# Optimization experiments

Hardware: AMD Instinct MI355X
Metric: run time of the kernel (lower is better)

The kernel has to match this reference:

```python
import jax, jax.numpy as jnp
import numpy as np

N = 4096          # num_nodes
E = 131072        # num_edges (avg degree 32)
H = 32            # hidden_channels
C_IN, C_OUT = 3, 3
DEPTH = 4
KS = [2000, 1000, 500, 250]  # ceil(ratio * n) per level, ratios = [2000/N, .5, .5, .5]


def gcn(x, A, W, b):
    """GCNConv with improved=True (self-loop fill 2, preserved if already present),
    symmetric normalization, aggregation out[dst] += norm * h[src]."""
    d = jnp.diagonal(A)
    A_hat = A + jnp.diag(jnp.where(d > 0, 0.0, 2.0))
    deg = A_hat.sum(0)                       # in-degree (col sums), as gcn_norm
    dis = jnp.where(deg > 0, jax.lax.rsqrt(deg), 0.0)
    msg = (x @ W) * dis[:, None]
    return (A_hat.T @ msg) * dis[:, None] + b


def augment(A):
    """GraphUNet.augment_adj: add self loops (w=1), square adjacency, drop self loops."""
    n = A.shape[0]
    eye = jnp.eye(n, dtype=A.dtype)
    A_sl = A + eye
    return (A_sl @ A_sl) * (1.0 - eye)


def pool(x, A, p, k):
    """TopKPooling: score = tanh((x.p)/||p||), keep top-k, gate x by score."""
    score = jnp.tanh((x @ p) / jnp.linalg.norm(p))
    vals, perm = jax.lax.top_k(score, k)
    return x[perm] * vals[:, None], A[perm][:, perm], perm


def setup_inputs() -> dict:
    key = jax.random.key(0)
    ks = jax.random.split(key, 12)
    x = jax.random.normal(ks[0], (N, C_IN), jnp.float32)
    edge_index = jax.random.randint(ks[1], (2, E), 0, N, dtype=jnp.int64)
    s = 0.1
    return {
        "x": x,
        "edge_index": edge_index,
        "W0": jax.random.normal(ks[2], (C_IN, H)) * s,
        "b0": jnp.zeros((H,), jnp.float32),
        "Wd": jax.random.normal(ks[3], (DEPTH, H, H)) * s,
        "bd": jnp.zeros((DEPTH, H), jnp.float32),
        "P": jax.random.normal(ks[4], (DEPTH, H)) * s,
        "Wu": jax.random.normal(ks[5], (DEPTH - 1, H, H)) * s,
        "bu": jnp.zeros((DEPTH - 1, H), jnp.float32),
        "Wlast": jax.random.normal(ks[6], (H, C_OUT)) * s,
        "blast": jnp.zeros((C_OUT,), jnp.float32),
    }


def reference(x, edge_index, W0, b0, Wd, bd, P, Wu, bu, Wlast, blast):
    # dense adjacency; duplicate edges accumulate like coalesced sparse weights
    A = jnp.zeros((N, N), jnp.float32).at[edge_index[0], edge_index[1]].add(1.0)
    x = jax.nn.relu(gcn(x, A, W0, b0))
    xs, As, perms = [x], [A], []
    for i in range(DEPTH):
        A = augment(A)
        x, A, perm = pool(x, A, P[i], KS[i])
        x = jax.nn.relu(gcn(x, A, Wd[i], bd[i]))
        if i < DEPTH - 1:
            xs.append(x)
            As.append(A)
        perms.append(perm)
    for i in range(DEPTH):
        j = DEPTH - 1 - i
        res = xs[j]
        up = jnp.zeros_like(res).at[perms[j]].set(x)  # unpool
        x = res + up                                   # sum_res=True
        if i < DEPTH - 1:
            x = jax.nn.relu(gcn(x, As[j], Wu[i], bu[i]))
        else:
            x = gcn(x, As[j], Wlast, blast)
    return jax.nn.log_softmax(x, axis=1)
```

## Files before the change

### kernel.cpp

```cpp
#include <hip/hip_runtime.h>
#include <math.h>

#define H 32
#define N0 4096
#define EMAX 131072
#define APSTR (4096 * 32)

typedef __attribute__((ext_vector_type(4))) float floatx4;
typedef __attribute__((ext_vector_type(8))) short short8;

__device__ __forceinline__ unsigned short f2bf_bits(float v) {
    union { float f; unsigned u; } c;
    c.f = v;
    unsigned lsb = (c.u >> 16) & 1u;
    c.u += 0x7fffu + lsb;
    return (unsigned short)(c.u >> 16);
}

__device__ __forceinline__ float bf2f(unsigned short u) {
    union { unsigned x; float f; } c;
    c.x = (unsigned)u << 16;
    return c.f;
}

__device__ __forceinline__ float cvtA(float f) { return f; }
__device__ __forceinline__ float cvtA(unsigned short u) { return bf2f(u); }

__global__ void fill_sentinel_kernel(float* out, int n) {
    int t = blockIdx.x * 256 + threadIdx.x;
    if (t < n) out[t] = 9.0f;
}

__global__ void build_stats_kernel(const int* __restrict__ ei, int E, int* __restrict__ rowcnt,
                                   int* __restrict__ rowcntD, int* __restrict__ diagcnt) {
    int t = blockIdx.x * 256 + threadIdx.x;
    if (t >= E) return;
    int s = ei[t], d = ei[E + t];
    if ((unsigned)s >= N0 || (unsigned)d >= N0) return;
    atomicAdd(&rowcnt[s], 1);
    atomicAdd(&rowcntD[d], 1);
    if (s == d) atomicAdd(&diagcnt[s], 1);
}

__global__ __launch_bounds__(1024) void scan2_kernel(const int* __restrict__ cntA, int* __restrict__ rowpA,
                                                     int* __restrict__ curA, const int* __restrict__ cntB,
                                                     int* __restrict__ rowpB, int* __restrict__ curB) {
    __shared__ int wsA[16], wsB[16], weA[16], weB[16];
    int tid = threadIdx.x;
    int lane = tid & 63, wid = tid >> 6;
    int base = tid * 4;
    int lA[4], lB[4];
    int sA = 0, sB = 0;
#pragma unroll
    for (int i = 0; i < 4; i++) { lA[i] = sA; sA += cntA[base + i]; }
#pragma unroll
    for (int i = 0; i < 4; i++) { lB[i] = sB; sB += cntB[base + i]; }
    int iA = sA, iB = sB;
#pragma unroll
    for (int off = 1; off < 64; off <<= 1) {
        int vA = __shfl_up(iA, off);
        int vB = __shfl_up(iB, off);
        if (lane >= off) { iA += vA; iB += vB; }
    }
    if (lane == 63) { wsA[wid] = iA; wsB[wid] = iB; }
    __syncthreads();
    if (tid < 16) {
        int a = wsA[tid], b = wsB[tid];
        int ia = a, ib = b;
#pragma unroll
        for (int off = 1; off < 16; off <<= 1) {
            int va = __shfl_up(ia, off);
            int vb = __shfl_up(ib, off);
            if (tid >= off) { ia += va; ib += vb; }
        }
        weA[tid] = ia - a;
        weB[tid] = ib - b;
    }
    __syncthreads();
    int preA = weA[wid] + iA - sA;
    int preB = weB[wid] + iB - sB;
#pragma unroll
    for (int i = 0; i < 4; i++) {
        int a = preA + lA[i], b = preB + lB[i];
        rowpA[base + i] = a; curA[base + i] = a;
        rowpB[base + i] = b; curB[base + i] = b;
    }
    if (tid == 1023) { rowpA[N0] = preA + sA; rowpB[N0] = preB + sB; }
}

__global__ void fillcsr_msg0_kernel(const int* __restrict__ ei, int E, int* __restrict__ cursor,
                                    int* __restrict__ cols, int* __restrict__ cursorD,
                                    int* __restrict__ srcs, const float* __restrict__ x,
                                    const float* __restrict__ Wb, const int* __restrict__ rcntD,
                                    const int* __restrict__ diagcnt, float* __restrict__ dis,
                                    float* __restrict__ fixb, float* __restrict__ msg, int n) {
    int nf = (E + 255) >> 8;
    int tid = threadIdx.x;
    if ((int)blockIdx.x < nf) {
        int t = blockIdx.x * 256 + tid;
        if (t >= E) return;
        int s = ei[t], d = ei[E + t];
        if ((unsigned)s >= N0 || (unsigned)d >= N0) return;
        int pos = atomicAdd(&cursor[s], 1);
        cols[pos] = d;
        int posD = atomicAdd(&cursorD[d], 1);
        srcs[posD] = s;
    } else {
        int idx = ((int)blockIdx.x - nf) * 256 + tid;
        if (idx >= n * 32) return;
        int i = idx >> 5, c = idx & 31;
        float fx = diagcnt[i] > 0 ? 0.f : 2.f;
        float dg = (float)rcntD[i] + fx;
        float di = dg > 0.f ? 1.f / sqrtf(dg) : 0.f;
        if (c == 0) { dis[i] = di; fixb[i] = fx; }
        float s = x[i * 3] * Wb[c] + x[i * 3 + 1] * Wb[32 + c] + x[i * 3 + 2] * Wb[64 + c];
        msg[idx] = s * di;
    }
}

__global__ __launch_bounds__(256) void aug0_kernel(const int* __restrict__ rowp, const int* __restrict__ cols,
                                                   const int* __restrict__ perm, const int* __restrict__ invperm,
                                                   int kOut, int ldC, unsigned short* __restrict__ C) {
    __shared__ float row[2048];
    int a = blockIdx.x;
    int tid = threadIdx.x;
    for (int j = tid; j < ldC; j += 256) row[j] = 0.f;
    __syncthreads();
    if (a < kOut) {
        int pa = perm[a];
        int s0 = rowp[pa], s1 = rowp[pa + 1];
        int sub = tid & 7, grp = tid >> 3;
        for (int e = s0 + grp; e < s1; e += 32) {
            int k = cols[e];
            if (sub == 0) {
                int ip = invperm[k];
                if (ip >= 0) atomicAdd(&row[ip], 2.0f);
            }
            int t1 = rowp[k + 1];
            for (int e2 = rowp[k] + sub; e2 < t1; e2 += 8) {
                int ip2 = invperm[cols[e2]];
                if (ip2 >= 0) atomicAdd(&row[ip2], 1.0f);
            }
        }
    }
    __syncthreads();
    for (int j = tid; j < ldC; j += 256)
        C[(long)a * ldC + j] = (j == a) ? 0 : f2bf_bits(row[j]);
}

__global__ void gatherAB_bf16_kernel(const unsigned short* __restrict__ M, int ldM,
                                     const int* __restrict__ perm, const int* __restrict__ invp,
                                     int kOut, unsigned short* __restrict__ Gr,
                                     unsigned short* __restrict__ GcT, int ldn,
                                     float* __restrict__ Cz) {
    __shared__ float t[32][33];
    __shared__ int rj[32];
    int half = (ldM >> 8) * ldn;
    int tseg = (ldM >> 5) * (ldM >> 5);
    int zrow = (((ldn - kOut) * ldM) + 255) >> 8;
    int u = blockIdx.x;
    int tid = threadIdx.x;
    if (u < half) {
        int gx = ldM >> 8;
        int a = u / gx;
        int k = (u % gx) * 256 + tid;
        float v = 0.f;
        if (a < kOut) {
            int pa = perm[a];
            v = bf2f(M[(long)pa * ldM + k]) + (k == pa ? 1.f : 0.f);
        }
        Gr[(long)a * ldM + k] = f2bf_bits(v);
    } else if (u < half + tseg) {
        u -= half;
        int ntx = ldM >> 5;
        int bx = u % ntx, by = u / ntx;
        int j0 = bx * 32, k0 = by * 32;
        int tx = tid & 31, ty = tid >> 5;
        if (ty == 0) rj[tx] = invp[j0 + tx];
        __syncthreads();
        for (int y = ty; y < 32; y += 8)
            t[y][tx] = bf2f(M[(long)(k0 + y) * ldM + j0 + tx]);
        __syncthreads();
        for (int y = ty; y < 32; y += 8) {
            int r = rj[y];
            if (r >= 0)
                GcT[(long)r * ldM + k0 + tx] =
                    f2bf_bits(t[tx][y] + ((k0 + tx) == (j0 + y) ? 1.f : 0.f));
        }
    } else if (u < half + tseg + zrow) {
        int e = (u - half - tseg) * 256 + tid;
        if (e < (ldn - kOut) * ldM) GcT[(long)kOut * ldM + e] = 0;
    } else {
        int t4 = (u - half - tseg - zrow) * 256 + tid;
        if (t4 < (ldn * ldn) >> 2) {
            floatx4 z = {0.f, 0.f, 0.f, 0.f};
            ((floatx4*)Cz)[t4] = z;
        }
    }
}

__global__ void gatherGT_kernel(const float* __restrict__ M, int ldM, const int* __restrict__ perm,
                                const int* __restrict__ invp, int kOut,
                                float* __restrict__ Gr, float* __restrict__ GcT, int ldn,
                                float* __restrict__ deg) {
    __shared__ float t[32][33];
    __shared__ int rj[32];
    int half = (ldM >> 8) * ldn;
    int tseg = (ldM >> 5) * (ldM >> 5);
    int zrow = (((ldn - kOut) * ldM) + 255) >> 8;
    int u = blockIdx.x;
    int tid = threadIdx.x;
    if (u < half) {
        int gx = ldM >> 8;
        int a = u / gx;
        int k = (u % gx) * 256 + tid;
        float v = 0.f;
        if (a < kOut) {
            int pa = perm[a];
            v = M[(long)pa * ldM + k] + (k == pa ? 1.f : 0.f);
        }
        Gr[(long)a * ldM + k] = v;
    } else if (u < half + tseg) {
        u -= half;
        int ntx = ldM >> 5;
        int bx = u % ntx, by = u / ntx;
        int j0 = bx * 32, k0 = by * 32;
        int tx = tid & 31, ty = tid >> 5;
        if (ty == 0) rj[tx] = invp[j0 + tx];
        __syncthreads();
        for (int y = ty; y < 32; y += 8)
            t[y][tx] = M[(long)(k0 + y) * ldM + j0 + tx];
        __syncthreads();
        for (int y = ty; y < 32; y += 8) {
            int r = rj[y];
            if (r >= 0)
                GcT[(long)r * ldM + k0 + tx] = t[tx][y] + ((k0 + tx) == (j0 + y) ? 1.f : 0.f);
        }
    } else if (u < half + tseg + zrow) {
        int e = (u - half - tseg) * 256 + tid;
        if (e < (ldn - kOut) * ldM) GcT[(long)kOut * ldM + e] = 0.f;
    } else {
        int tt = (u - half - tseg - zrow) * 256 + tid;
        if (tt < ldn) deg[tt] = 0.f;
    }
}

__global__ __launch_bounds__(256) void mfma_aug_kernel(const unsigned short* __restrict__ Aop,
                                                       const unsigned short* __restrict__ Bop,
                                                       float* __restrict__ C, int K, int ldC, int kchunk) {
    __shared__ __align__(16) unsigned short lA[64 * 32];
    __shared__ __align__(16) unsigned short lB[64 * 32];
    const int tid = threadIdx.x;
    const int lane = tid & 63;
    const int w = tid >> 6;
    const int a0 = blockIdx.y * 64, b0 = blockIdx.x * 64;
    const int kbase = blockIdx.z * kchunk;
    const int r0 = tid >> 2;
    const int c8 = (tid & 3) * 8;
    const unsigned short* gA = Aop + (long)(a0 + r0) * K + kbase + c8;
    const unsigned short* gB = Bop + (long)(b0 + r0) * K + kbase + c8;
    const int wm = (w & 1) * 32;
    const int wn = (w >> 1) * 32;
    const int lm = lane & 15;
    const int quad = lane >> 4;
    floatx4 acc[2][2];
#pragma unroll
    for (int i = 0; i < 2; i++)
#pragma unroll
        for (int j = 0; j < 2; j++) {
            floatx4 z = {0.f, 0.f, 0.f, 0.f};
            acc[i][j] = z;
        }
    for (int k0 = 0; k0 < kchunk; k0 += 32) {
        short8 va = *(const short8*)(gA + k0);
        short8 vb = *(const short8*)(gB + k0);
        __syncthreads();
        *(short8*)&lA[r0 * 32 + c8] = va;
        *(short8*)&lB[r0 * 32 + c8] = vb;
        __syncthreads();
        short8 af[2], bf[2];
#pragma unroll
        for (int mi = 0; mi < 2; mi++) af[mi] = *(const short8*)&lA[(wm + mi * 16 + lm) * 32 + quad * 8];
#pragma unroll
        for (int ni = 0; ni < 2; ni++) bf[ni] = *(const short8*)&lB[(wn + ni * 16 + lm) * 32 + quad * 8];
#pragma unroll
        for (int mi = 0; mi < 2; mi++)
#pragma unroll
            for (int ni = 0; ni < 2; ni++)
                acc[mi][ni] = __builtin_amdgcn_mfma_f32_16x16x32_bf16(af[mi], bf[ni], acc[mi][ni], 0, 0, 0);
    }
#pragma unroll
    for (int mi = 0; mi < 2; mi++)
#pragma unroll
        for (int ni = 0; ni < 2; ni++) {
            int col = b0 + wn + ni * 16 + lm;
#pragma unroll
            for (int r = 0; r < 4; r++) {
                int row = a0 + wm + mi * 16 + quad * 4 + r;
                if (row != col) atomicAdd(&C[(long)row * ldC + col], acc[mi][ni][r]);
            }
        }
}

__global__ __launch_bounds__(256) void gemm64_kernel(const float* __restrict__ Gr,
                                                     const float* __restrict__ GcT,
                                                     float* __restrict__ Cpart, int K, int ldC, int kchunk) {
    __shared__ float As[32][68];
    __shared__ float Bs[32][68];
    const int tid = threadIdx.x;
    const int a0 = blockIdx.y * 64, b0 = blockIdx.x * 64;
    const int kbase = blockIdx.z * kchunk;
    float* Cz = Cpart + (long)blockIdx.z * ldC * ldC;
    const int tx = tid & 15, ty = tid >> 4;
    const int lr = tid >> 2;
    const int lk = (tid & 3) * 8;
    const float* gA = Gr + (long)(a0 + lr) * K + lk + kbase;
    const float* gB = GcT + (long)(b0 + lr) * K + lk + kbase;
    float acc[4][4];
#pragma unroll
    for (int i = 0; i < 4; i++)
#pragma unroll
        for (int j = 0; j < 4; j++) acc[i][j] = 0.f;
    for (int k0 = 0; k0 < kchunk; k0 += 32) {
        float a8[8], b8[8];
#pragma unroll
        for (int i = 0; i < 8; i++) a8[i] = gA[k0 + i];
#pragma unroll
        for (int i = 0; i < 8; i++) b8[i] = gB[k0 + i];
        __syncthreads();
#pragma unroll
        for (int i = 0; i < 8; i++) As[lk + i][lr] = a8[i];
#pragma unroll
        for (int i = 0; i < 8; i++) Bs[lk + i][lr] = b8[i];
        __syncthreads();
#pragma unroll
        for (int k = 0; k < 32; k++) {
            floatx4 av = *(const floatx4*)&As[k][ty * 4];
            floatx4 bv = *(const floatx4*)&Bs[k][tx * 4];
#pragma unroll
            for (int i = 0; i < 4; i++)
#pragma unroll
                for (int j = 0; j < 4; j++) acc[i][j] += av[i] * bv[j];
        }
    }
#pragma unroll
    for (int i = 0; i < 4; i++)
#pragma unroll
        for (int j = 0; j < 4; j++) {
            int a = a0 + ty * 4 + i, b = b0 + tx * 4 + j;
            Cz[(long)a * ldC + b] = acc[i][j];
        }
}

__global__ void reduce_part_deg_kernel(const float* __restrict__ Cpart, float* __restrict__ C,
                                       int ldC, int ksplit, float* __restrict__ deg) {
    int t = blockIdx.x * 256 + threadIdx.x;
    long tot = (long)ldC * ldC;
    if (t >= tot) return;
    float s = 0.f;
    for (int z = 0; z < ksplit; z++) s += Cpart[(long)z * tot + t];
    int a = t / ldC, b = t % ldC;
    if (a == b) s = 0.f;
    C[t] = s;
    if (s != 0.f) atomicAdd(&deg[b], s);
}

template <typename AT>
__global__ void colsum_rawmsg_kernel(const AT* __restrict__ A, int ld, int hascs,
                                     const float* __restrict__ x, const int* __restrict__ perm,
                                     const float* __restrict__ vals, const float* __restrict__ xup,
                                     const int* __restrict__ invp, const float* __restrict__ Wb,
                                     float* __restrict__ degp, float* __restrict__ rm, int n) {
    int nc = hascs ? (ld >> 8) * (ld >> 6) : 0;
    int tid = threadIdx.x;
    if ((int)blockIdx.x < nc) {
        int gx = ld >> 8;
        int bi = blockIdx.x % gx, jb = blockIdx.x / gx;
        int i = bi * 256 + tid;
        int j0 = jb * 64;
        const AT* p = A + (long)j0 * ld + i;
        float s0 = 0.f, s1 = 0.f, s2 = 0.f, s3 = 0.f, s4 = 0.f, s5 = 0.f, s6 = 0.f, s7 = 0.f;
#pragma unroll
        for (int jq = 0; jq < 64; jq += 8) {
            float v[8];
#pragma unroll
            for (int q = 0; q < 8; q++) v[q] = cvtA(p[(long)(jq + q) * ld]);
            s0 += v[0]; s1 += v[1]; s2 += v[2]; s3 += v[3];
            s4 += v[4]; s5 += v[5]; s6 += v[6]; s7 += v[7];
        }
        float s = ((s0 + s1) + (s2 + s3)) + ((s4 + s5) + (s6 + s7));
        degp[(long)jb * ld + i] = s;
    } else {
        int idx = ((int)blockIdx.x - nc) * 256 + tid;
        if (idx >= ld * 32) return;
        int i = idx >> 5, c = idx & 31;
        float v = 0.f;
        if (i < n) {
            int src = perm ? perm[i] : i;
            float vs = vals ? vals[i] : 1.f;
            int ip = invp ? invp[i] : -1;
            float s = 0.f;
#pragma unroll
            for (int q = 0; q < 32; q++) {
                float xv = x[(long)src * 32 + q];
                if (ip >= 0) xv += xup[(long)ip * 32 + q];
                s += xv * Wb[q * 32 + c];
            }
            v = s * vs;
        }
        rm[idx] = v;
    }
}

template <typename AT>
__global__ __launch_bounds__(256) void aggTs_kernel(const AT* __restrict__ A,
                                                    const float* __restrict__ rm,
                                                    const float* __restrict__ degp, int nparts,
                                                    const float* __restrict__ disC,
                                                    float* __restrict__ aggp, int n, int ld, int jchunk) {
    __shared__ float As[64][64];
    __shared__ float Ms[64][32];
    __shared__ float sdisJ[256];
    const int tid = threadIdx.x;
    const int i0 = blockIdx.x * 64;
    const int j0 = blockIdx.y * jchunk;
    for (int j = tid; j < jchunk; j += 256) {
        int jj = j0 + j;
        float d;
        if (nparts) {
            float s = 0.f;
            for (int z = 0; z < nparts; z++) s += degp[(long)z * ld + jj];
            d = 1.f / sqrtf(s + 2.f);
        } else {
            d = disC[jj];
        }
        sdisJ[j] = d;
    }
    __syncthreads();
    const int il = tid & 63;
    const int cg = tid >> 6;
    const int i = i0 + il;
    const int mrow = tid >> 2;
    const int mc = (tid & 3) * 8;
    float acc[8];
#pragma unroll
    for (int q = 0; q < 8; q++) acc[q] = 0.f;
    for (int jb = j0; jb < j0 + jchunk; jb += 64) {
        AT a16[16];
        float m8[8];
#pragma unroll
        for (int q = 0; q < 16; q++) a16[q] = A[(long)(jb + cg + 4 * q) * ld + i0 + il];
#pragma unroll
        for (int q = 0; q < 8; q++) m8[q] = rm[(long)(jb + mrow) * 32 + mc + q];
        __syncthreads();
#pragma unroll
        for (int q = 0; q < 16; q++) As[cg + 4 * q][il] = cvtA(a16[q]);
        float ds = sdisJ[jb - j0 + mrow];
#pragma unroll
        for (int q = 0; q < 8; q++) Ms[mrow][mc + q] = m8[q] * ds;
        __syncthreads();
#pragma unroll
        for (int jl = 0; jl < 64; jl++) {
            float a = As[jl][il];
#pragma unroll
            for (int q = 0; q < 8; q++) acc[q] += a * Ms[jl][cg * 8 + q];
        }
        __syncthreads();
    }
    if (i < n) {
#pragma unroll
        for (int q = 0; q < 8; q++) aggp[(long)blockIdx.y * APSTR + (long)i * 32 + cg * 8 + q] = acc[q];
    }
}

__global__ void epi2_kernel(const float* __restrict__ aggp, int jsplit, const float* __restrict__ rm,
                            const float* __restrict__ degp, int nparts, float* __restrict__ disC,
                            int writeDis, int ld, const float* __restrict__ bb,
                            float* __restrict__ out, int n, const float* __restrict__ p, int npow,
                            unsigned long long* __restrict__ keys) {
    __shared__ float psh[32];
    if (p) {
        if (threadIdx.x < 32) psh[threadIdx.x] = p[threadIdx.x];
        __syncthreads();
    }
    int idx = blockIdx.x * 256 + threadIdx.x;
    int tot = (p ? npow : n) * 32;
    if (idx >= tot) return;
    int i = idx >> 5, c = idx & 31;
    float di;
    if (nparts) {
        float s = 0.f;
        for (int z = 0; z < nparts; z++) s += degp[(long)z * ld + i];
        di = 1.f / sqrtf(s + 2.f);
    } else {
        di = disC[i];
    }
    float v = 0.f;
    if (i < n) {
        float s = 0.f;
        for (int z = 0; z < jsplit; z++) s += aggp[(long)z * APSTR + idx];
        v = (s + 2.f * di * rm[idx]) * di + bb[c];
        v = fmaxf(v, 0.f);
        out[idx] = v;
    }
    if (writeDis && c == 0) disC[i] = di;
    if (p) {
        float pc = psh[c];
        float d = v * pc;
        float nq = pc * pc;
#pragma unroll
        for (int st = 16; st >= 1; st >>= 1) {
            d += __shfl_xor(d, st);
            nq += __shfl_xor(nq, st);
        }
        if (c == 0) {
            unsigned long long kk = 0ULL;
            if (i < n) {
                float sc = tanhf(d / sqrtf(nq));
                unsigned u = __float_as_uint(sc);
                u = (u & 0x80000000u) ? ~u : (u | 0x80000000u);
                kk = ((unsigned long long)u << 32) | (unsigned)(~i);
            }
            keys[i] = kk;
        }
    }
}

__global__ void cscagg_epi_keys_kernel(const int* __restrict__ rowpD, const int* __restrict__ srcs,
                                       const float* __restrict__ msg, const float* __restrict__ dis,
                                       const float* __restrict__ fixb, const float* __restrict__ bb,
                                       float* __restrict__ out, int n, const float* __restrict__ p,
                                       unsigned long long* __restrict__ keys) {
    __shared__ float psh[32];
    if (threadIdx.x < 32) psh[threadIdx.x] = p[threadIdx.x];
    __syncthreads();
    int idx = blockIdx.x * 256 + threadIdx.x;
    if (idx >= n * 32) return;
    int i = idx >> 5, c = idx & 31;
    float acc = 0.f;
    int e0 = rowpD[i], e1 = rowpD[i + 1];
    for (int e = e0; e < e1; e++) acc += msg[(long)srcs[e] * 32 + c];
    float v = (acc + fixb[i] * msg[idx]) * dis[i] + bb[c];
    v = fmaxf(v, 0.f);
    out[idx] = v;
    float pc = psh[c];
    float d = v * pc;
    float nq = pc * pc;
#pragma unroll
    for (int st = 16; st >= 1; st >>= 1) {
        d += __shfl_xor(d, st);
        nq += __shfl_xor(nq, st);
    }
    if (c == 0) {
        float sc = tanhf(d / sqrtf(nq));
        unsigned u = __float_as_uint(sc);
        u = (u & 0x80000000u) ? ~u : (u | 0x80000000u);
        keys[i] = ((unsigned long long)u << 32) | (unsigned)(~i);
    }
}

__global__ void msg3up_kernel(const float* __restrict__ res, const float* __restrict__ xup,
                              const int* __restrict__ invp, const float* __restrict__ Wb,
                              const float* __restrict__ dis, float* __restrict__ msg, int n) {
    int idx = blockIdx.x * 256 + threadIdx.x;
    if (idx >= n * 3) return;
    int i = idx / 3, c = idx % 3;
    int ip = invp[i];
    float s = 0.f;
#pragma unroll
    for (int q = 0; q < 32; q++) {
        float xv = res[(long)i * 32 + q];
        if (ip >= 0) xv += xup[(long)ip * 32 + q];
        s += xv * Wb[q * 3 + c];
    }
    msg[idx] = s * dis[i];
}

__global__ void cscagg_lsm_kernel(const int* __restrict__ rowpD, const int* __restrict__ srcs,
                                  const float* __restrict__ msg, const float* __restrict__ dis,
                                  const float* __restrict__ fixb, const float* __restrict__ bb,
                                  float* __restrict__ out, int n) {
    int i = blockIdx.x * 256 + threadIdx.x;
    if (i >= n) return;
    float a0 = 0.f, a1 = 0.f, a2 = 0.f;
    int e0 = rowpD[i], e1 = rowpD[i + 1];
    for (int e = e0; e < e1; e++) {
        const float* m = &msg[(long)srcs[e] * 3];
        a0 += m[0]; a1 += m[1]; a2 += m[2];
    }
    float di = dis[i], fx = fixb[i];
    float v0 = (a0 + fx * msg[i * 3]) * di + bb[0];
    float v1 = (a1 + fx * msg[i * 3 + 1]) * di + bb[1];
    float v2 = (a2 + fx * msg[i * 3 + 2]) * di + bb[2];
    float m = fmaxf(v0, fmaxf(v1, v2));
    float s = expf(v0 - m) + expf(v1 - m) + expf(v2 - m);
    float l = m + logf(s);
    out[i * 3] = v0 - l;
    out[i * 3 + 1] = v1 - l;
    out[i * 3 + 2] = v2 - l;
}

__global__ __launch_bounds__(256) void topk_rank_kernel(const unsigned long long* __restrict__ keys,
                                                        int npow, int k, int* __restrict__ perm,
                                                        float* __restrict__ vals,
                                                        int* __restrict__ invperm) {
    __shared__ unsigned long long ks[4096];
    __shared__ int psum[256];
    const int tid = threadIdx.x;
    for (int t = tid; t < npow; t += 256) ks[t] = keys[t];
    __syncthreads();
    const int m = tid & 15;
    const int chunk = tid >> 4;
    const int myi = blockIdx.x * 16 + m;
    unsigned long long my = ks[myi];
    const int cl = npow >> 4;
    const unsigned long long* base = &ks[chunk * cl];
    int r = 0;
#pragma unroll 4
    for (int j = 0; j < cl; j++) r += (base[j] > my) ? 1 : 0;
    psum[chunk * 16 + m] = r;
    __syncthreads();
    if (tid < 16) {
        int mk_i = blockIdx.x * 16 + tid;
        unsigned long long mk = ks[mk_i];
        int rank = 0;
#pragma unroll
        for (int c = 0; c < 16; c++) rank += psum[c * 16 + tid];
        invperm[mk_i] = (rank < k) ? rank : -1;
        if (rank < k) {
            perm[rank] = (int)(~(unsigned)mk);
            unsigned u = (unsigned)(mk >> 32);
            u = (u & 0x80000000u) ? (u ^ 0x80000000u) : ~u;
            vals[rank] = __uint_as_float(u);
        }
    }
}

static void run_dense(hipStream_t st, const void* A, int abf, int n, int ld, const float* x,
                      const int* perm, const float* vals, const float* xup, const int* invp,
                      const float* Wt, const float* bt, float* out,
                      float* degp, int nparts, int hascs, float* disC, int writeDis,
                      float* aggp, float* rm,
                      const float* pnext, int npow, unsigned long long* keys) {
    {
        int nc = hascs ? (ld >> 8) * (ld >> 6) : 0;
        int g = nc + (ld * 32 + 255) / 256;
        if (abf)
            colsum_rawmsg_kernel<unsigned short><<<g, 256, 0, st>>>(
                (const unsigned short*)A, ld, hascs, x, perm, vals, xup, invp, Wt, degp, rm, n);
        else
            colsum_rawmsg_kernel<float><<<g, 256, 0, st>>>(
                (const float*)A, ld, hascs, x, perm, vals, xup, invp, Wt, degp, rm, n);
    }
    int jsplit = (ld >= 256) ? (ld >> 8) : 1;
    if (jsplit < 1) jsplit = 1;
    int jchunk = ld / jsplit;
    dim3 ga(ld / 64, jsplit);
    if (abf)
        aggTs_kernel<unsigned short><<<ga, 256, 0, st>>>((const unsigned short*)A, rm,
                                                         nparts ? degp : nullptr, nparts, disC,
                                                         aggp, n, ld, jchunk);
    else
        aggTs_kernel<float><<<ga, 256, 0, st>>>((const float*)A, rm, nparts ? degp : nullptr,
                                                nparts, disC, aggp, n, ld, jchunk);
    int gme = ((pnext ? npow : n) * 32 + 255) / 256;
    epi2_kernel<<<gme, 256, 0, st>>>(aggp, jsplit, rm, nparts ? degp : nullptr, nparts, disC,
                                     writeDis, ld, bt, out, n, pnext, npow, keys);
}

extern "C" void kernel_launch(void* const* d_in, const int* in_sizes, int n_in,
                              void* d_out, int out_size, void* d_ws, size_t ws_size,
                              hipStream_t stream) {
    const float* x0f = (const float*)d_in[0];
    const int* eidx = (const int*)d_in[1];
    const float* W0f = (const float*)d_in[2];
    const float* b0f = (const float*)d_in[3];
    const float* Wdf = (const float*)d_in[4];
    const float* bdf = (const float*)d_in[5];
    const float* Pf = (const float*)d_in[6];
    const float* Wuf = (const float*)d_in[7];
    const float* buf2 = (const float*)d_in[8];
    const float* Wlf = (const float*)d_in[9];
    const float* blf = (const float*)d_in[10];
    const int E = in_sizes[1] / 2;

    unsigned char* w = (unsigned char*)d_ws;
    size_t off = 0;
    auto alloc = [&](size_t bytes) -> void* {
        void* p = w + off;
        off += (bytes + 255) & ~(size_t)255;
        return p;
    };
    int* rowcnt = (int*)alloc(N0 * 4);
    int* rowcntD = (int*)alloc(N0 * 4);
    int* diagcnt = (int*)alloc(N0 * 4);
    int* rowp = (int*)alloc((N0 + 1) * 4);
    int* rowpD = (int*)alloc((N0 + 1) * 4);
    int* cursor = (int*)alloc(N0 * 4);
    int* cursorD = (int*)alloc(N0 * 4);
    int* cols = (int*)alloc((size_t)EMAX * 4);
    int* srcs = (int*)alloc((size_t)EMAX * 4);
    float* dis0 = (float*)alloc(N0 * 4);
    float* fixb0 = (float*)alloc(N0 * 4);
    unsigned long long* keys = (unsigned long long*)alloc((size_t)N0 * 8);
    unsigned short* A1 = (unsigned short*)alloc((size_t)2048 * 2048 * 2);
    float* A2 = (float*)alloc((size_t)1024 * 1024 * 4);
    float* A3 = (float*)alloc((size_t)512 * 512 * 4);
    float* A4 = (float*)alloc((size_t)256 * 256 * 4);
    float* Gr = (float*)alloc((size_t)1024 * 2048 * 4);
    float* Gc = (float*)alloc((size_t)2048 * 1024 * 4);
    unsigned short* Grb = (unsigned short*)alloc((size_t)1024 * 2048 * 2);
    unsigned short* GcTb = (unsigned short*)alloc((size_t)1024 * 2048 * 2);
    float* Cpart = (float*)alloc((size_t)8 * 512 * 512 * 4);
    float* degp = (float*)alloc((size_t)32 * 2048 * 4);
    float* aggp = (float*)alloc((size_t)8 * APSTR * 4);
    float* xs0 = (float*)alloc((size_t)N0 * H * 4);
    float* xs1 = (float*)alloc((size_t)2000 * H * 4);
    float* xs2 = (float*)alloc((size_t)1000 * H * 4);
    float* xs3 = (float*)alloc((size_t)500 * H * 4);
    float* xtB = (float*)alloc((size_t)N0 * H * 4);
    float* xtC = (float*)alloc((size_t)N0 * H * 4);
    float* msgb = (float*)alloc((size_t)N0 * H * 4);
    float* disL = (float*)alloc((size_t)4 * N0 * 4);
    int* invpermL = (int*)alloc((size_t)4 * N0 * 4);
    const int ksz[4] = {2000, 1000, 500, 250};
    int* perm[4];
    float* vals[4];
    for (int i = 0; i < 4; i++) perm[i] = (int*)alloc((size_t)ksz[i] * 4);
    for (int i = 0; i < 4; i++) vals[i] = (float*)alloc((size_t)ksz[i] * 4);

    if (off > ws_size) {
        fill_sentinel_kernel<<<(out_size + 255) / 256, 256, 0, stream>>>((float*)d_out, out_size);
        return;
    }

    const int nlvl[5] = {N0, 2000, 1000, 500, 250};
    const int ldl[5] = {N0, 2048, 1024, 512, 256};
    const int npw[4] = {4096, 2048, 1024, 512};
    void* Afp[5] = {nullptr, A1, A2, A3, A4};
    const int abfL[5] = {0, 1, 0, 0, 0};
    float* xsb[4] = {xs0, xs1, xs2, xs3};

    hipMemsetAsync(rowcnt, 0, (size_t)N0 * 3 * 4, stream);
    build_stats_kernel<<<(E + 255) / 256, 256, 0, stream>>>(eidx, E, rowcnt, rowcntD, diagcnt);
    scan2_kernel<<<1, 1024, 0, stream>>>(rowcnt, rowp, cursor, rowcntD, rowpD, cursorD);
    {
        int nf = (E + 255) / 256;
        int nm = (N0 * H + 255) / 256;
        fillcsr_msg0_kernel<<<nf + nm, 256, 0, stream>>>(eidx, E, cursor, cols, cursorD, srcs,
                                                         x0f, W0f, rowcntD, diagcnt, dis0, fixb0,
                                                         msgb, N0);
    }
    cscagg_epi_keys_kernel<<<(N0 * H + 255) / 256, 256, 0, stream>>>(rowpD, srcs, msgb, dis0, fixb0,
                                                                     b0f, xs0, N0, Pf, keys);
    float* xcur = xs0;

    for (int i = 0; i < 4; ++i) {
        int kk = ksz[i], ldn = ldl[i + 1];
        topk_rank_kernel<<<npw[i] / 16, 256, 0, stream>>>(keys, npw[i], kk, perm[i], vals[i],
                                                          invpermL + i * N0);
        if (i == 0) {
            aug0_kernel<<<ldn, 256, 0, stream>>>(rowp, cols, perm[0], invpermL, kk, ldn, A1);
        } else if (i == 1) {
            int ldM = ldl[i];
            int half = (ldM >> 8) * ldn;
            int tseg = (ldM >> 5) * (ldM >> 5);
            int zrow = (((ldn - kk) * ldM) + 255) >> 8;
            int zseg = ((ldn * ldn) / 4 + 255) / 256;
            gatherAB_bf16_kernel<<<half + tseg + zrow + zseg, 256, 0, stream>>>(
                A1, ldM, perm[i], invpermL + i * N0, kk, Grb, GcTb, ldn, A2);
            int ksplit = 2;
            int kchunk = ldM / ksplit;
            dim3 gg(ldn / 64, ldn / 64, ksplit);
            mfma_aug_kernel<<<gg, 256, 0, stream>>>(Grb, GcTb, A2, ldM, ldn, kchunk);
        } else {
            int ldM = ldl[i];
            int half = (ldM >> 8) * ldn;
            int tseg = (ldM >> 5) * (ldM >> 5);
            int zrow = (((ldn - kk) * ldM) + 255) >> 8;
            int dseg = (ldn + 255) / 256;
            gatherGT_kernel<<<half + tseg + zrow + dseg, 256, 0, stream>>>(
                (const float*)Afp[i], ldM, perm[i], invpermL + i * N0, kk, Gr, Gc, ldn, degp);
            int ksplit = 8;
            int kchunk = ldM / ksplit;
            dim3 gg(ldn / 64, ldn / 64, ksplit);
            gemm64_kernel<<<gg, 256, 0, stream>>>(Gr, Gc, Cpart, ldM, ldn, kchunk);
            long tot = (long)ldn * ldn;
            reduce_part_deg_kernel<<<(tot + 255) / 256, 256, 0, stream>>>(Cpart, (float*)Afp[i + 1],
                                                                          ldn, ksplit, degp);
        }
        float* outx = (i < 3) ? xsb[i + 1] : xtB;
        const float* pnext = (i < 3) ? (Pf + (i + 1) * H) : nullptr;
        int npown = (i < 3) ? npw[i + 1] : 0;
        int hascs = (i <= 1) ? 1 : 0;
        int nparts = (i <= 1) ? (ldn >> 6) : 1;
        run_dense(stream, Afp[i + 1], abfL[i + 1], kk, ldn, xcur, perm[i], vals[i], nullptr,
                  nullptr, Wdf + i * (H * H), bdf + i * H, outx, degp, nparts, hascs,
                  disL + i * N0, (i < 3) ? 1 : 0, aggp, msgb, pnext, npown, keys);
        xcur = outx;
    }

    for (int i = 0; i < 4; ++i) {
        int j = 3 - i;
        int nj = nlvl[j];
        if (i < 3) {
            int ldn = ldl[j];
            float* outx = (xcur == xtB) ? xtC : xtB;
            run_dense(stream, Afp[j], abfL[j], nj, ldn, xsb[j], nullptr, nullptr, xcur,
                      invpermL + j * N0, Wuf + i * (H * H), buf2 + i * H, outx, nullptr, 0, 0,
                      disL + (j - 1) * N0, 0, aggp, msgb, nullptr, 0, nullptr);
            xcur = outx;
        } else {
            msg3up_kernel<<<(N0 * 3 + 255) / 256, 256, 0, stream>>>(xs0, xcur, invpermL, Wlf, dis0,
                                                                    msgb, N0);
            cscagg_lsm_kernel<<<(N0 + 255) / 256, 256, 0, stream>>>(rowpD, srcs, msgb, dis0, fixb0,
                                                                    blf, (float*)d_out, N0);
        }
    }
}
```

Before: 421.1 us.

## Fuse row gather into augment GEMMs and replace split-K reduce with atomics

The augment GEMMs now read rows of the previous adjacency directly through the perm index, adding the self-loop inside the load, so the gathered row matrix Gr/Grb no longer has to be materialised. For levels 2-3 the split-K partial buffer and the separate reduce kernel are dropped. Instead the GEMM atomically accumulates into a pre-zeroed output and computes per-column degree partials in shared memory. This saves a kernel launch and a round trip through memory per level, at the cost of atomic contention and a non-deterministic summation order.

New measurement: 432.6 us. 2.7% more time.

```diff
diff --git a/kernel.cpp b/kernel.cpp
--- a/kernel.cpp
+++ b/kernel.cpp
@@ -148,30 +148,17 @@
         C[(long)a * ldC + j] = (j == a) ? 0 : f2bf_bits(row[j]);
 }
 
-__global__ void gatherAB_bf16_kernel(const unsigned short* __restrict__ M, int ldM,
-                                     const int* __restrict__ perm, const int* __restrict__ invp,
-                                     int kOut, unsigned short* __restrict__ Gr,
-                                     unsigned short* __restrict__ GcT, int ldn,
-                                     float* __restrict__ Cz) {
+__global__ void gatherABt_bf16_kernel(const unsigned short* __restrict__ M, int ldM,
+                                      const int* __restrict__ invp, int kOut,
+                                      unsigned short* __restrict__ GcT, int ldn,
+                                      float* __restrict__ Cz) {
     __shared__ float t[32][33];
     __shared__ int rj[32];
-    int half = (ldM >> 8) * ldn;
     int tseg = (ldM >> 5) * (ldM >> 5);
     int zrow = (((ldn - kOut) * ldM) + 255) >> 8;
     int u = blockIdx.x;
     int tid = threadIdx.x;
-    if (u < half) {
-        int gx = ldM >> 8;
-        int a = u / gx;
-        int k = (u % gx) * 256 + tid;
-        float v = 0.f;
-        if (a < kOut) {
-            int pa = perm[a];
-            v = bf2f(M[(long)pa * ldM + k]) + (k == pa ? 1.f : 0.f);
-        }
-        Gr[(long)a * ldM + k] = f2bf_bits(v);
-    } else if (u < half + tseg) {
-        u -= half;
+    if (u < tseg) {
         int ntx = ldM >> 5;
         int bx = u % ntx, by = u / ntx;
         int j0 = bx * 32, k0 = by * 32;
@@ -187,11 +174,11 @@
                 GcT[(long)r * ldM + k0 + tx] =
                     f2bf_bits(t[tx][y] + ((k0 + tx) == (j0 + y) ? 1.f : 0.f));
         }
-    } else if (u < half + tseg + zrow) {
-        int e = (u - half - tseg) * 256 + tid;
+    } else if (u < tseg + zrow) {
+        int e = (u - tseg) * 256 + tid;
         if (e < (ldn - kOut) * ldM) GcT[(long)kOut * ldM + e] = 0;
     } else {
-        int t4 = (u - half - tseg - zrow) * 256 + tid;
+        int t4 = (u - tseg - zrow) * 256 + tid;
         if (t4 < (ldn * ldn) >> 2) {
             floatx4 z = {0.f, 0.f, 0.f, 0.f};
             ((floatx4*)Cz)[t4] = z;
@@ -199,29 +186,18 @@
     }
 }
 
-__global__ void gatherGT_kernel(const float* __restrict__ M, int ldM, const int* __restrict__ perm,
-                                const int* __restrict__ invp, int kOut,
-                                float* __restrict__ Gr, float* __restrict__ GcT, int ldn,
-                                float* __restrict__ deg) {
+__global__ void gatherT_kernel(const float* __restrict__ M, int ldM,
+                               const int* __restrict__ invp, int kOut,
+                               float* __restrict__ GcT, int ldn,
+                               float* __restrict__ Cz, float* __restrict__ deg) {
     __shared__ float t[32][33];
     __shared__ int rj[32];
-    int half = (ldM >> 8) * ldn;
     int tseg = (ldM >> 5) * (ldM >> 5);
     int zrow = (((ldn - kOut) * ldM) + 255) >> 8;
+    int zcseg = ((ldn * ldn) / 4 + 255) / 256;
     int u = blockIdx.x;
     int tid = threadIdx.x;
-    if (u < half) {
-        int gx = ldM >> 8;
-        int a = u / gx;
-        int k = (u % gx) * 256 + tid;
-        float v = 0.f;
-        if (a < kOut) {
-            int pa = perm[a];
-            v = M[(long)pa * ldM + k] + (k == pa ? 1.f : 0.f);
-        }
-        Gr[(long)a * ldM + k] = v;
-    } else if (u < half + tseg) {
-        u -= half;
+    if (u < tseg) {
         int ntx = ldM >> 5;
         int bx = u % ntx, by = u / ntx;
         int j0 = bx * 32, k0 = by * 32;
@@ -236,16 +212,23 @@
             if (r >= 0)
                 GcT[(long)r * ldM + k0 + tx] = t[tx][y] + ((k0 + tx) == (j0 + y) ? 1.f : 0.f);
         }
-    } else if (u < half + tseg + zrow) {
-        int e = (u - half - tseg) * 256 + tid;
+    } else if (u < tseg + zrow) {
+        int e = (u - tseg) * 256 + tid;
         if (e < (ldn - kOut) * ldM) GcT[(long)kOut * ldM + e] = 0.f;
+    } else if (u < tseg + zrow + zcseg) {
+        int t4 = (u - tseg - zrow) * 256 + tid;
+        if (t4 < (ldn * ldn) >> 2) {
+            floatx4 z = {0.f, 0.f, 0.f, 0.f};
+            ((floatx4*)Cz)[t4] = z;
+        }
     } else {
-        int tt = (u - half - tseg - zrow) * 256 + tid;
+        int tt = (u - tseg - zrow - zcseg) * 256 + tid;
         if (tt < ldn) deg[tt] = 0.f;
     }
 }
 
-__global__ __launch_bounds__(256) void mfma_aug_kernel(const unsigned short* __restrict__ Aop,
+__global__ __launch_bounds__(256) void mfma_aug_kernel(const unsigned short* __restrict__ A1,
+                                                       const int* __restrict__ perm, int kOut,
                                                        const unsigned short* __restrict__ Bop,
                                                        float* __restrict__ C, int K, int ldC, int kchunk) {
     __shared__ __align__(16) unsigned short lA[64 * 32];
@@ -257,7 +240,9 @@
     const int kbase = blockIdx.z * kchunk;
     const int r0 = tid >> 2;
     const int c8 = (tid & 3) * 8;
-    const unsigned short* gA = Aop + (long)(a0 + r0) * K + kbase + c8;
+    const int arow = a0 + r0;
+    const int pa = (arow < kOut) ? perm[arow] : -1;
+    const unsigned short* gA = A1 + (pa >= 0 ? (long)pa * K : 0) + kbase + c8;
     const unsigned short* gB = Bop + (long)(b0 + r0) * K + kbase + c8;
     const int wm = (w & 1) * 32;
     const int wn = (w >> 1) * 32;
@@ -272,7 +257,18 @@
             acc[i][j] = z;
         }
     for (int k0 = 0; k0 < kchunk; k0 += 32) {
-        short8 va = *(const short8*)(gA + k0);
+        short8 va;
+        if (pa >= 0) {
+            va = *(const short8*)(gA + k0);
+            int cb = kbase + c8 + k0;
+            if (pa >= cb && pa < cb + 8) {
+                int e = pa - cb;
+                va[e] = (short)f2bf_bits(bf2f((unsigned short)va[e]) + 1.0f);
+            }
+        } else {
+            short8 z = {0, 0, 0, 0, 0, 0, 0, 0};
+            va = z;
+        }
         short8 vb = *(const short8*)(gB + k0);
         __syncthreads();
         *(short8*)&lA[r0 * 32 + c8] = va;
@@ -302,19 +298,22 @@
         }
 }
 
-__global__ __launch_bounds__(256) void gemm64_kernel(const float* __restrict__ Gr,
-                                                     const float* __restrict__ GcT,
-                                                     float* __restrict__ Cpart, int K, int ldC, int kchunk) {
+__global__ __launch_bounds__(256) void gemm64_atomic_kernel(const float* __restrict__ A,
+                                                            const int* __restrict__ perm, int kOut,
+                                                            const float* __restrict__ GcT,
+                                                            float* __restrict__ C, float* __restrict__ deg,
+                                                            int K, int ldC, int kchunk) {
     __shared__ float As[32][68];
     __shared__ float Bs[32][68];
     const int tid = threadIdx.x;
     const int a0 = blockIdx.y * 64, b0 = blockIdx.x * 64;
     const int kbase = blockIdx.z * kchunk;
-    float* Cz = Cpart + (long)blockIdx.z * ldC * ldC;
     const int tx = tid & 15, ty = tid >> 4;
     const int lr = tid >> 2;
     const int lk = (tid & 3) * 8;
-    const float* gA = Gr + (long)(a0 + lr) * K + lk + kbase;
+    const int arow = a0 + lr;
+    const int pa = (arow < kOut) ? perm[arow] : -1;
+    const float* gA = A + (pa >= 0 ? (long)pa * K : 0) + lk + kbase;
     const float* gB = GcT + (long)(b0 + lr) * K + lk + kbase;
     float acc[4][4];
 #pragma unroll
@@ -323,8 +322,15 @@
         for (int j = 0; j < 4; j++) acc[i][j] = 0.f;
     for (int k0 = 0; k0 < kchunk; k0 += 32) {
         float a8[8], b8[8];
-#pragma unroll
-        for (int i = 0; i < 8; i++) a8[i] = gA[k0 + i];
+        if (pa >= 0) {
+#pragma unroll
+            for (int i = 0; i < 8; i++) a8[i] = gA[k0 + i];
+            int cb = kbase + lk + k0;
+            if (pa >= cb && pa < cb + 8) a8[pa - cb] += 1.f;
+        } else {
+#pragma unroll
+            for (int i = 0; i < 8; i++) a8[i] = 0.f;
+        }
 #pragma unroll
         for (int i = 0; i < 8; i++) b8[i] = gB[k0 + i];
         __syncthreads();
@@ -343,26 +349,28 @@
                 for (int j = 0; j < 4; j++) acc[i][j] += av[i] * bv[j];
         }
     }
+    __syncthreads();
+    float* cps = &As[0][0];
+    float cloc[4] = {0.f, 0.f, 0.f, 0.f};
 #pragma unroll
     for (int i = 0; i < 4; i++)
 #pragma unroll
         for (int j = 0; j < 4; j++) {
             int a = a0 + ty * 4 + i, b = b0 + tx * 4 + j;
-            Cz[(long)a * ldC + b] = acc[i][j];
-        }
-}
-
-__global__ void reduce_part_deg_kernel(const float* __restrict__ Cpart, float* __restrict__ C,
-                                       int ldC, int ksplit, float* __restrict__ deg) {
-    int t = blockIdx.x * 256 + threadIdx.x;
-    long tot = (long)ldC * ldC;
-    if (t >= tot) return;
-    float s = 0.f;
-    for (int z = 0; z < ksplit; z++) s += Cpart[(long)z * tot + t];
-    int a = t / ldC, b = t % ldC;
-    if (a == b) s = 0.f;
-    C[t] = s;
-    if (s != 0.f) atomicAdd(&deg[b], s);
+            float v = acc[i][j];
+            if (a != b) {
+                if (v != 0.f) atomicAdd(&C[(long)a * ldC + b], v);
+                cloc[j] += v;
+            }
+        }
+#pragma unroll
+    for (int j = 0; j < 4; j++) cps[ty * 68 + tx * 4 + j] = cloc[j];
+    __syncthreads();
+    if (tid < 64) {
+        float s = 0.f;
+        for (int t = 0; t < 16; t++) s += cps[t * 68 + tid];
+        if (s != 0.f) atomicAdd(&deg[b0 + tid], s);
+    }
 }
 
 template <typename AT>
@@ -707,11 +715,8 @@
     float* A2 = (float*)alloc((size_t)1024 * 1024 * 4);
     float* A3 = (float*)alloc((size_t)512 * 512 * 4);
     float* A4 = (float*)alloc((size_t)256 * 256 * 4);
-    float* Gr = (float*)alloc((size_t)1024 * 2048 * 4);
     float* Gc = (float*)alloc((size_t)2048 * 1024 * 4);
-    unsigned short* Grb = (unsigned short*)alloc((size_t)1024 * 2048 * 2);
     unsigned short* GcTb = (unsigned short*)alloc((size_t)1024 * 2048 * 2);
-    float* Cpart = (float*)alloc((size_t)8 * 512 * 512 * 4);
     float* degp = (float*)alloc((size_t)32 * 2048 * 4);
     float* aggp = (float*)alloc((size_t)8 * APSTR * 4);
     float* xs0 = (float*)alloc((size_t)N0 * H * 4);
@@ -763,31 +768,30 @@
             aug0_kernel<<<ldn, 256, 0, stream>>>(rowp, cols, perm[0], invpermL, kk, ldn, A1);
         } else if (i == 1) {
             int ldM = ldl[i];
-            int half = (ldM >> 8) * ldn;
             int tseg = (ldM >> 5) * (ldM >> 5);
             int zrow = (((ldn - kk) * ldM) + 255) >> 8;
             int zseg = ((ldn * ldn) / 4 + 255) / 256;
-            gatherAB_bf16_kernel<<<half + tseg + zrow + zseg, 256, 0, stream>>>(
-                A1, ldM, perm[i], invpermL + i * N0, kk, Grb, GcTb, ldn, A2);
+            gatherABt_bf16_kernel<<<tseg + zrow + zseg, 256, 0, stream>>>(
+                A1, ldM, invpermL + i * N0, kk, GcTb, ldn, A2);
             int ksplit = 2;
             int kchunk = ldM / ksplit;
             dim3 gg(ldn / 64, ldn / 64, ksplit);
-            mfma_aug_kernel<<<gg, 256, 0, stream>>>(Grb, GcTb, A2, ldM, ldn, kchunk);
+            mfma_aug_kernel<<<gg, 256, 0, stream>>>(A1, perm[i], kk, GcTb, A2, ldM, ldn, kchunk);
         } else {
             int ldM = ldl[i];
-            int half = (ldM >> 8) * ldn;
             int tseg = (ldM >> 5) * (ldM >> 5);
             int zrow = (((ldn - kk) * ldM) + 255) >> 8;
+            int zcseg = ((ldn * ldn) / 4 + 255) / 256;
             int dseg = (ldn + 255) / 256;
-            gatherGT_kernel<<<half + tseg + zrow + dseg, 256, 0, stream>>>(
-                (const float*)Afp[i], ldM, perm[i], invpermL + i * N0, kk, Gr, Gc, ldn, degp);
+            gatherT_kernel<<<tseg + zrow + zcseg + dseg, 256, 0, stream>>>(
+                (const float*)Afp[i], ldM, invpermL + i * N0, kk, Gc, ldn,
+                (float*)Afp[i + 1], degp);
             int ksplit = 8;
             int kchunk = ldM / ksplit;
             dim3 gg(ldn / 64, ldn / 64, ksplit);
-            gemm64_kernel<<<gg, 256, 0, stream>>>(Gr, Gc, Cpart, ldM, ldn, kchunk);
-            long tot = (long)ldn * ldn;
-            reduce_part_deg_kernel<<<(tot + 255) / 256, 256, 0, stream>>>(Cpart, (float*)Afp[i + 1],
-                                                                          ldn, ksplit, degp);
+            gemm64_atomic_kernel<<<gg, 256, 0, stream>>>((const float*)Afp[i], perm[i], kk, Gc,
+                                                         (float*)Afp[i + 1], degp, ldM, ldn,
+                                                         kchunk);
         }
         float* outx = (i < 3) ? xsb[i + 1] : xtB;
         const float* pnext = (i < 3) ? (Pf + (i + 1) * H) : nullptr;
```
